# Optimization experiments

Measured on AMD Instinct MI355X. Metric: run time of the kernel, lower is better.

The kernel has to match this reference:

```python
import jax, jax.numpy as jnp
import numpy as np

EMBD = 1024
N_HEADS = 16
DK = EMBD // N_HEADS


def setup_inputs() -> dict:
    key = jax.random.key(0)
    ks = jax.random.split(key, 5)
    B, T = 2, 2048
    scale = 1.0 / np.sqrt(EMBD)
    x = jax.random.normal(ks[0], (B, T, EMBD), dtype=jnp.float32)
    W_qkv = jax.random.normal(ks[1], (EMBD, 3 * EMBD), dtype=jnp.float32) * scale
    b_qkv = jnp.zeros((3 * EMBD,), dtype=jnp.float32)
    W_proj = jax.random.normal(ks[2], (EMBD, EMBD), dtype=jnp.float32) * scale
    b_proj = jnp.zeros((EMBD,), dtype=jnp.float32)
    return {"x": x, "W_qkv": W_qkv, "b_qkv": b_qkv, "W_proj": W_proj, "b_proj": b_proj}


def reference(x, W_qkv, b_qkv, W_proj, b_proj):
    B, T, C = x.shape
    qkv = x @ W_qkv + b_qkv                      # [B, T, 3C]
    q, k, v = jnp.split(qkv, 3, axis=-1)
    # [B, H, T, dk]
    q = q.reshape(B, T, N_HEADS, DK).transpose(0, 2, 1, 3)
    k = k.reshape(B, T, N_HEADS, DK).transpose(0, 2, 1, 3)
    v = v.reshape(B, T, N_HEADS, DK).transpose(0, 2, 1, 3)
    att = jnp.einsum('bhqd,bhkd->bhqk', q, k) / np.sqrt(DK).astype(np.float32)
    causal = jnp.triu(jnp.full((T, T), -jnp.inf, dtype=att.dtype), k=1)
    att = jax.nn.softmax(att + causal, axis=-1)  # dropout p=0.0 -> identity
    y = jnp.einsum('bhqk,bhkd->bhqd', att, v)    # [B, H, T, dk]
    y = y.transpose(0, 2, 1, 3).reshape(B, T, C)
    y = y @ W_proj + b_proj
    return (y, (k, v))
```

## Files before the change

### kernel.cpp

```cpp
#include <hip/hip_runtime.h>
#include <hip/hip_bf16.h>

#define B_   2
#define T_   2048
#define C_   1024
#define H_   16
#define DK_  64

typedef __bf16 bf16x8 __attribute__((ext_vector_type(8)));
typedef __bf16 bf16x4v __attribute__((ext_vector_type(4)));
typedef float  f32x4  __attribute__((ext_vector_type(4)));
typedef unsigned short u16;
typedef u16 u16x4 __attribute__((ext_vector_type(4)));
typedef u16 u16x8 __attribute__((ext_vector_type(8)));

static __device__ __forceinline__ u16 f2bf(float f) {
    unsigned u = __float_as_uint(f);
    u += 0x7fffu + ((u >> 16) & 1u);
    return (u16)(u >> 16);
}
static __device__ __forceinline__ float bf2f(u16 h) {
    return __uint_as_float(((unsigned)h) << 16);
}

static __device__ __forceinline__ void async16(void* l, const void* g) {
    __builtin_amdgcn_global_load_lds(
        (const __attribute__((address_space(1))) unsigned int*)g,
        (__attribute__((address_space(3))) unsigned int*)l, 16, 0, 0);
}

__global__ __launch_bounds__(256) void pack_a_hl(const float* __restrict__ src, char* __restrict__ dst) {
    const int mt = blockIdx.x, kt = blockIdx.y, t = threadIdx.x;
    const int r = t >> 1, half = t & 1;
    const float* s = src + (size_t)(mt * 128 + r) * 1024 + kt * 32 + half * 16;
    float f[16];
    #pragma unroll
    for (int i = 0; i < 4; ++i) *(float4*)&f[i * 4] = ((const float4*)s)[i];
    u16 hi[16] __attribute__((aligned(16))), lo[16] __attribute__((aligned(16)));
    #pragma unroll
    for (int e = 0; e < 16; ++e) { hi[e] = f2bf(f[e]); lo[e] = f2bf(f[e] - bf2f(hi[e])); }
    char* tb = dst + ((size_t)mt * 32 + kt) * 16384;
    const int sw = (r & 7) << 4;
    #pragma unroll
    for (int j = 0; j < 2; ++j) {
        int g = half * 2 + j;
        *(u16x8*)(tb + ((r * 128 + g * 16) ^ sw))      = *(u16x8*)&hi[j * 8];
        *(u16x8*)(tb + ((r * 128 + 64 + g * 16) ^ sw)) = *(u16x8*)&lo[j * 8];
    }
}

__global__ __launch_bounds__(256) void pack_a_s(const float* __restrict__ src, char* __restrict__ dst) {
    const int mt = blockIdx.x, kt = blockIdx.y, t = threadIdx.x;
    const int r = t >> 1, half = t & 1;
    const float* s = src + (size_t)(mt * 128 + r) * 1024 + kt * 64 + half * 32;
    float f[32];
    #pragma unroll
    for (int i = 0; i < 8; ++i) *(float4*)&f[i * 4] = ((const float4*)s)[i];
    u16 hv[32] __attribute__((aligned(16)));
    #pragma unroll
    for (int e = 0; e < 32; ++e) hv[e] = f2bf(f[e]);
    char* tb = dst + ((size_t)mt * 16 + kt) * 16384;
    const int sw = (r & 7) << 4;
    #pragma unroll
    for (int j = 0; j < 4; ++j) {
        int g = half * 4 + j;
        *(u16x8*)(tb + ((r * 128 + g * 16) ^ sw)) = *(u16x8*)&hv[j * 8];
    }
}

template <int BKT>
__global__ __launch_bounds__(256) void pack_bt_hl(const float* __restrict__ W, char* __restrict__ dst,
                                                  int N, int nkt) {
    __shared__ float Ls[BKT][132];
    const int nt = blockIdx.x, kt = blockIdx.y, t = threadIdx.x;
    #pragma unroll
    for (int p = 0; p < BKT / 32; ++p) {
        int kr = p * 32 + (t >> 3), c8 = t & 7;
        const float* s = W + (size_t)(kt * BKT + kr) * N + nt * 128 + c8 * 16;
        #pragma unroll
        for (int i = 0; i < 4; ++i) *(float4*)&Ls[kr][c8 * 16 + i * 4] = ((const float4*)s)[i];
    }
    __syncthreads();
    const int nr = t >> 1, half = t & 1;
    constexpr int KH = BKT / 2;
    constexpr int ROWB = BKT * 4;
    constexpr int TILEB = 128 * ROWB;
    char* tb = dst + ((size_t)nt * nkt + kt) * TILEB;
    u16 hi[KH] __attribute__((aligned(16))), lo[KH] __attribute__((aligned(16)));
    #pragma unroll
    for (int e = 0; e < KH; ++e) {
        float x = Ls[half * KH + e][nr];
        hi[e] = f2bf(x); lo[e] = f2bf(x - bf2f(hi[e]));
    }
    const int sw = (nr & 7) << 4;
    #pragma unroll
    for (int j = 0; j < KH / 8; ++j) {
        int g = half * (KH / 8) + j;
        *(u16x8*)(tb + ((nr * ROWB + g * 16) ^ sw))            = *(u16x8*)&hi[j * 8];
        *(u16x8*)(tb + ((nr * ROWB + ROWB / 2 + g * 16) ^ sw)) = *(u16x8*)&lo[j * 8];
    }
}

__global__ __launch_bounds__(256) void kv_pack(
    const float* __restrict__ k_in, const float* __restrict__ v_in,
    char* __restrict__ kp, char* __restrict__ vp)
{
    __shared__ float Ls[64][68];
    const int bh = blockIdx.x, kt = blockIdx.y, t = threadIdx.x;
    const float* Kb = k_in + (size_t)bh * T_ * DK_ + (size_t)kt * 64 * DK_;
    const float* Vb = v_in + (size_t)bh * T_ * DK_ + (size_t)kt * 64 * DK_;
    char* ktb = kp + ((size_t)bh * 32 + kt) * 16384;
    char* vtb = vp + ((size_t)bh * 32 + kt) * 16384;
    const int row = t >> 2, qtr = t & 3;

    {
        float f[16];
        #pragma unroll
        for (int i = 0; i < 4; ++i)
            *(float4*)&f[i * 4] = ((const float4*)(Kb + (size_t)row * 64 + qtr * 16))[i];
        u16 hi[16] __attribute__((aligned(16))), lo[16] __attribute__((aligned(16)));
        #pragma unroll
        for (int e = 0; e < 16; ++e) { hi[e] = f2bf(f[e]); lo[e] = f2bf(f[e] - bf2f(hi[e])); }
        const int sw = (row & 7) << 4;
        *(u16x8*)(ktb + ((row * 128 + qtr * 32) ^ sw))             = *(u16x8*)&hi[0];
        *(u16x8*)(ktb + ((row * 128 + qtr * 32 + 16) ^ sw))        = *(u16x8*)&hi[8];
        *(u16x8*)(ktb + 8192 + ((row * 128 + qtr * 32) ^ sw))      = *(u16x8*)&lo[0];
        *(u16x8*)(ktb + 8192 + ((row * 128 + qtr * 32 + 16) ^ sw)) = *(u16x8*)&lo[8];
    }

    #pragma unroll
    for (int i = 0; i < 4; ++i)
        *(float4*)&Ls[row][qtr * 16 + i * 4] = ((const float4*)(Vb + (size_t)row * 64 + qtr * 16))[i];
    __syncthreads();
    {
        const int dd = t >> 2, tc2 = t & 3;
        float f[16];
        #pragma unroll
        for (int k = 0; k < 16; ++k) f[k] = Ls[tc2 * 16 + k][dd];
        u16 hi[16] __attribute__((aligned(16))), lo[16] __attribute__((aligned(16)));
        #pragma unroll
        for (int e = 0; e < 16; ++e) { hi[e] = f2bf(f[e]); lo[e] = f2bf(f[e] - bf2f(hi[e])); }
        const int sw = (dd & 7) << 4;
        *(u16x8*)(vtb + ((dd * 128 + tc2 * 32) ^ sw))             = *(u16x8*)&hi[0];
        *(u16x8*)(vtb + ((dd * 128 + tc2 * 32 + 16) ^ sw))        = *(u16x8*)&hi[8];
        *(u16x8*)(vtb + 8192 + ((dd * 128 + tc2 * 32) ^ sw))      = *(u16x8*)&lo[0];
        *(u16x8*)(vtb + 8192 + ((dd * 128 + tc2 * 32 + 16) ^ sw)) = *(u16x8*)&lo[8];
    }
}

__global__ __launch_bounds__(256, 2) void qkv_gemm_bf16(
    const char* __restrict__ xp, const char* __restrict__ wqp,
    const float* __restrict__ bqkv,
    float* __restrict__ qy, float* __restrict__ k_out, float* __restrict__ v_out)
{
    __shared__ __align__(16) char Alds[16384];
    __shared__ __align__(16) char Blds[16384];
    const int mt = blockIdx.x, nt = blockIdx.y;
    const int t = threadIdx.x, lane = t & 63, w = t >> 6;
    const int g = lane >> 4, r15 = lane & 15;
    const int wm = w >> 1, wn = w & 1;

    int aoff[4][2], boff[4][2];
    #pragma unroll
    for (int s = 0; s < 4; ++s) {
        int ar = wm * 64 + s * 16 + r15, sa = (ar & 7) << 4;
        aoff[s][0] = (ar * 128 + g * 16) ^ sa;
        aoff[s][1] = (ar * 128 + 64 + g * 16) ^ sa;
        int br = wn * 64 + s * 16 + r15, sb = (br & 7) << 4;
        boff[s][0] = (br * 128 + g * 16) ^ sb;
        boff[s][1] = (br * 128 + 64 + g * 16) ^ sb;
    }

    f32x4 acc[4][4];
    #pragma unroll
    for (int i = 0; i < 4; ++i)
        #pragma unroll
        for (int j = 0; j < 4; ++j) acc[i][j] = (f32x4){0.f, 0.f, 0.f, 0.f};

    const char* Abase = xp + (size_t)mt * 32 * 16384 + w * 4096 + lane * 16;
    const char* Bbase = wqp + (size_t)nt * 32 * 16384 + w * 4096 + lane * 16;
    char* la = Alds + w * 4096;
    char* lb = Blds + w * 4096;

    for (int kt = 0; kt < 32; ++kt) {
        #pragma unroll
        for (int i = 0; i < 4; ++i) {
            async16(la + i * 1024, Abase + kt * 16384 + i * 1024);
            async16(lb + i * 1024, Bbase + kt * 16384 + i * 1024);
        }
        __syncthreads();
        bf16x8 af[4][2], bf[4][2];
        #pragma unroll
        for (int s = 0; s < 4; ++s) {
            af[s][0] = *(const bf16x8*)(Alds + aoff[s][0]);
            af[s][1] = *(const bf16x8*)(Alds + aoff[s][1]);
            bf[s][0] = *(const bf16x8*)(Blds + boff[s][0]);
            bf[s][1] = *(const bf16x8*)(Blds + boff[s][1]);
        }
        #pragma unroll
        for (int i = 0; i < 4; ++i)
            #pragma unroll
            for (int j = 0; j < 4; ++j) {
                acc[i][j] = __builtin_amdgcn_mfma_f32_16x16x32_bf16(af[i][0], bf[j][0], acc[i][j], 0, 0, 0);
                acc[i][j] = __builtin_amdgcn_mfma_f32_16x16x32_bf16(af[i][0], bf[j][1], acc[i][j], 0, 0, 0);
                acc[i][j] = __builtin_amdgcn_mfma_f32_16x16x32_bf16(af[i][1], bf[j][0], acc[i][j], 0, 0, 0);
            }
        __syncthreads();
    }

    const int n0 = nt * 128;
    const int sec = n0 >> 10;
    float* kv = (sec == 1) ? k_out : v_out;
    #pragma unroll
    for (int i = 0; i < 4; ++i) {
        int mbase = mt * 128 + wm * 64 + i * 16 + g * 4;
        #pragma unroll
        for (int j = 0; j < 4; ++j) {
            int n = n0 + wn * 64 + j * 16 + r15;
            float bias = bqkv[n];
            int c = n & 1023;
            #pragma unroll
            for (int r = 0; r < 4; ++r) {
                int m = mbase + r;
                int bb = m >> 11, tt = m & 2047;
                float val = acc[i][j][r] + bias;
                if (sec == 0)
                    qy[((size_t)bb * T_ + tt) * C_ + c] = val;
                else
                    kv[(((size_t)bb * H_ + (c >> 6)) * T_ + tt) * DK_ + (c & 63)] = val;
            }
        }
    }
}

__global__ __launch_bounds__(256, 2) void proj_gemm_bf16(
    const char* __restrict__ yap, const char* __restrict__ wpp,
    const float* __restrict__ bp, float* __restrict__ y)
{
    __shared__ __align__(16) char Alds[16384];
    __shared__ __align__(16) char Blds[32768];
    const int mt = blockIdx.x, nt = blockIdx.y;
    const int t = threadIdx.x, lane = t & 63, w = t >> 6;
    const int g = lane >> 4, r15 = lane & 15;
    const int wm = w >> 1, wn = w & 1;

    int aoff[4][2], boffh[4][2], boffl[4][2];
    #pragma unroll
    for (int s = 0; s < 4; ++s) {
        int ar = wm * 64 + s * 16 + r15, sa = (ar & 7) << 4;
        int br = wn * 64 + s * 16 + r15, sb = (br & 7) << 4;
        #pragma unroll
        for (int kk = 0; kk < 2; ++kk) {
            aoff[s][kk]  = (ar * 128 + (kk * 4 + g) * 16) ^ sa;
            boffh[s][kk] = (br * 256 + (kk * 4 + g) * 16) ^ sb;
            boffl[s][kk] = (br * 256 + 128 + (kk * 4 + g) * 16) ^ sb;
        }
    }

    f32x4 acc[4][4];
    #pragma unroll
    for (int i = 0; i < 4; ++i)
        #pragma unroll
        for (int j = 0; j < 4; ++j) acc[i][j] = (f32x4){0.f, 0.f, 0.f, 0.f};

    const char* Abase = yap + (size_t)mt * 16 * 16384 + w * 4096 + lane * 16;
    const char* Bbase = wpp + (size_t)nt * 16 * 32768 + w * 8192 + lane * 16;
    char* la = Alds + w * 4096;
    char* lb = Blds + w * 8192;

    for (int kt = 0; kt < 16; ++kt) {
        #pragma unroll
        for (int i = 0; i < 4; ++i)
            async16(la + i * 1024, Abase + kt * 16384 + i * 1024);
        #pragma unroll
        for (int i = 0; i < 8; ++i)
            async16(lb + i * 1024, Bbase + kt * 32768 + i * 1024);
        __syncthreads();
        #pragma unroll
        for (int kk = 0; kk < 2; ++kk) {
            bf16x8 af[4], bh[4], bl[4];
            #pragma unroll
            for (int s = 0; s < 4; ++s) {
                af[s] = *(const bf16x8*)(Alds + aoff[s][kk]);
                bh[s] = *(const bf16x8*)(Blds + boffh[s][kk]);
                bl[s] = *(const bf16x8*)(Blds + boffl[s][kk]);
            }
            #pragma unroll
            for (int i = 0; i < 4; ++i)
                #pragma unroll
                for (int j = 0; j < 4; ++j) {
                    acc[i][j] = __builtin_amdgcn_mfma_f32_16x16x32_bf16(af[i], bh[j], acc[i][j], 0, 0, 0);
                    acc[i][j] = __builtin_amdgcn_mfma_f32_16x16x32_bf16(af[i], bl[j], acc[i][j], 0, 0, 0);
                }
        }
        __syncthreads();
    }

    #pragma unroll
    for (int i = 0; i < 4; ++i) {
        int mbase = mt * 128 + wm * 64 + i * 16 + g * 4;
        #pragma unroll
        for (int j = 0; j < 4; ++j) {
            int n = nt * 128 + wn * 64 + j * 16 + r15;
            float bias = bp[n];
            #pragma unroll
            for (int r = 0; r < 4; ++r)
                y[(size_t)(mbase + r) * 1024 + n] = acc[i][j][r] + bias;
        }
    }
}

#define PS_   0
#define KS_H  8192
#define KS_L  16384
#define VT_H  24576
#define VT_L  32768

__global__ __launch_bounds__(256) void attn_mfma_kernel(
    float* qyatt,
    const char* __restrict__ Kp,
    const char* __restrict__ Vp)
{
    __shared__ __align__(16) char lds[40960];

    const int bh   = blockIdx.x;
    const int qt   = 31 - (int)blockIdx.y;
    const int qb   = qt * 64;
    const int t    = threadIdx.x;
    const int lane = t & 63;
    const int w    = t >> 6;
    const int g    = lane >> 4;
    const int r15  = lane & 15;
    const int b    = bh >> 4, h = bh & 15;

    const float* Qb = qyatt + ((size_t)b * T_ + qb) * C_ + h * 64;
    const float QSCALE = 0.125f * 1.44269504088896f;

    #pragma unroll
    for (int di = 0; di < 4; ++di) {
        int fidx = di * 256 + t;
        int row  = fidx >> 4;
        int c4   = fidx & 15;
        float4 f = ((const float4*)(Qb + (size_t)row * C_))[c4];
        f.x *= QSCALE; f.y *= QSCALE; f.z *= QSCALE; f.w *= QSCALE;
        u16 h0 = f2bf(f.x), h1 = f2bf(f.y), h2 = f2bf(f.z), h3 = f2bf(f.w);
        u16 l0 = f2bf(f.x - bf2f(h0)), l1 = f2bf(f.y - bf2f(h1));
        u16 l2 = f2bf(f.z - bf2f(h2)), l3 = f2bf(f.w - bf2f(h3));
        int off = (row * 128 + c4 * 8) ^ ((row & 7) << 4);
        u16x4 hv = {h0, h1, h2, h3};
        u16x4 lv = {l0, l1, l2, l3};
        *(u16x4*)(lds + PS_  + off) = hv;
        *(u16x4*)(lds + KS_H + off) = lv;
    }
    __syncthreads();

    bf16x8 qfh[2], qfl[2];
    const int prow = w * 16 + r15;
    #pragma unroll
    for (int dc = 0; dc < 2; ++dc) {
        int off = (prow * 128 + dc * 64 + g * 16) ^ ((prow & 7) << 4);
        qfh[dc] = *(const bf16x8*)(lds + PS_  + off);
        qfl[dc] = *(const bf16x8*)(lds + KS_H + off);
    }

    f32x4 zero4 = {0.f, 0.f, 0.f, 0.f};
    f32x4 o[4];
    o[0] = zero4; o[1] = zero4; o[2] = zero4; o[3] = zero4;
    float mrun = -1e30f, lrun = 0.f;
    const int qglob = qb + w * 16 + r15;

    const int nt = qt + 1;
    for (int kt = 0; kt < nt; ++kt) {
        const int j0 = kt * 64;
        __syncthreads();
        {
            const char* Kg = Kp + ((size_t)bh * 32 + kt) * 16384 + w * 4096 + lane * 16;
            const char* Vg = Vp + ((size_t)bh * 32 + kt) * 16384 + w * 4096 + lane * 16;
            char* lk = lds + KS_H + w * 4096;
            char* lv = lds + VT_H + w * 4096;
            #pragma unroll
            for (int i = 0; i < 4; ++i) {
                async16(lk + i * 1024, Kg + i * 1024);
                async16(lv + i * 1024, Vg + i * 1024);
            }
        }
        __syncthreads();

        float sv[4][4];
        const bool diag = (kt == qt);
        #pragma unroll
        for (int st = 0; st < 4; ++st) {
            f32x4 acc = zero4;
            int krow = st * 16 + r15;
            #pragma unroll
            for (int dc = 0; dc < 2; ++dc) {
                int off = (krow * 128 + dc * 64 + g * 16) ^ ((krow & 7) << 4);
                bf16x8 kh = *(const bf16x8*)(lds + KS_H + off);
                bf16x8 kl = *(const bf16x8*)(lds + KS_L + off);
                acc = __builtin_amdgcn_mfma_f32_16x16x32_bf16(kh, qfh[dc], acc, 0, 0, 0);
                acc = __builtin_amdgcn_mfma_f32_16x16x32_bf16(kh, qfl[dc], acc, 0, 0, 0);
                acc = __builtin_amdgcn_mfma_f32_16x16x32_bf16(kl, qfh[dc], acc, 0, 0, 0);
            }
            #pragma unroll
            for (int r = 0; r < 4; ++r) {
                float x = acc[r];
                if (diag) {
                    int kg = j0 + st * 16 + g * 4 + r;
                    if (kg > qglob) x = -1e30f;
                }
                sv[st][r] = x;
            }
        }

        float tm = sv[0][0];
        #pragma unroll
        for (int st = 0; st < 4; ++st)
            #pragma unroll
            for (int r = 0; r < 4; ++r) tm = fmaxf(tm, sv[st][r]);
        tm = fmaxf(tm, __shfl_xor(tm, 16));
        tm = fmaxf(tm, __shfl_xor(tm, 32));
        if (__any(tm > mrun + 11.5f)) {
            float mnew = fmaxf(mrun, tm);
            float resc = exp2f(mrun - mnew);
            mrun = mnew;
            lrun *= resc;
            o[0] *= resc; o[1] *= resc; o[2] *= resc; o[3] *= resc;
        }

        float ps = 0.f;
        #pragma unroll
        for (int st = 0; st < 4; ++st)
            #pragma unroll
            for (int r = 0; r < 4; ++r) {
                float p = exp2f(sv[st][r] - mrun);
                sv[st][r] = p;
                ps += p;
            }
        ps += __shfl_xor(ps, 16);
        ps += __shfl_xor(ps, 32);
        lrun += ps;

        #pragma unroll
        for (int st = 0; st < 4; ++st) {
            bf16x4v pb = { (__bf16)sv[st][0], (__bf16)sv[st][1],
                           (__bf16)sv[st][2], (__bf16)sv[st][3] };
            int off = (prow * 128 + (st * 16 + g * 4) * 2) ^ ((prow & 7) << 4);
            *(bf16x4v*)(lds + PS_ + off) = pb;
        }

        bf16x8 pf[2];
        #pragma unroll
        for (int kc = 0; kc < 2; ++kc) {
            int off = (prow * 128 + kc * 64 + g * 16) ^ ((prow & 7) << 4);
            pf[kc] = *(const bf16x8*)(lds + PS_ + off);
        }
        #pragma unroll
        for (int dt = 0; dt < 4; ++dt) {
            int vrow = dt * 16 + r15;
            #pragma unroll
            for (int kc = 0; kc < 2; ++kc) {
                int off = (vrow * 128 + kc * 64 + g * 16) ^ ((vrow & 7) << 4);
                bf16x8 vh = *(const bf16x8*)(lds + VT_H + off);
                bf16x8 vl = *(const bf16x8*)(lds + VT_L + off);
                o[dt] = __builtin_amdgcn_mfma_f32_16x16x32_bf16(vh, pf[kc], o[dt], 0, 0, 0);
                o[dt] = __builtin_amdgcn_mfma_f32_16x16x32_bf16(vl, pf[kc], o[dt], 0, 0, 0);
            }
        }
    }

    const float inv = 1.f / lrun;
    float* yo = qyatt + ((size_t)b * T_ + qglob) * C_ + h * DK_;
    #pragma unroll
    for (int dt = 0; dt < 4; ++dt)
        #pragma unroll
        for (int r = 0; r < 4; ++r)
            yo[dt * 16 + g * 4 + r] = o[dt][r] * inv;
}

extern "C" void kernel_launch(void* const* d_in, const int* in_sizes, int n_in,
                              void* d_out, int out_size, void* d_ws, size_t ws_size,
                              hipStream_t stream) {
    const float* x     = (const float*)d_in[0];
    const float* Wqkv  = (const float*)d_in[1];
    const float* bqkv  = (const float*)d_in[2];
    const float* Wproj = (const float*)d_in[3];
    const float* bproj = (const float*)d_in[4];

    float* y     = (float*)d_out;
    float* k_out = y + (size_t)4194304;
    float* v_out = y + (size_t)8388608;

    char* ws = (char*)d_ws;
    char* xp  = ws;
    char* wqp = ws + ((size_t)16 << 20);
    char* Kp  = ws;
    char* Vp  = ws + ((size_t)16 << 20);
    char* yap = ws;
    char* wpp = ws + ((size_t)8 << 20);

    pack_a_hl     <<<dim3(32, 32), 256, 0, stream>>>(x, xp);
    pack_bt_hl<32><<<dim3(24, 32), 256, 0, stream>>>(Wqkv, wqp, 3072, 32);
    qkv_gemm_bf16 <<<dim3(32, 24), 256, 0, stream>>>(xp, wqp, bqkv, y, k_out, v_out);
    kv_pack       <<<dim3(32, 32), 256, 0, stream>>>(k_out, v_out, Kp, Vp);
    attn_mfma_kernel<<<dim3(32, 32), 256, 0, stream>>>(y, Kp, Vp);
    pack_a_s      <<<dim3(32, 16), 256, 0, stream>>>(y, yap);
    pack_bt_hl<64><<<dim3(8, 16), 256, 0, stream>>>(Wproj, wpp, 1024, 16);
    proj_gemm_bf16<<<dim3(32, 8), 256, 0, stream>>>(yap, wpp, bproj, y);
}
```

Before: 298.7 us.

## Double-buffer K/V tiles and widen attention blocks to 128 query rows

The attention kernel now processes 128 query rows per block with 8 waves, so each K/V tile loaded into LDS is shared by twice as many queries. K/V tiles are double-buffered: the next tile's async copy is issued before computing on the current one, leaving one barrier per iteration instead of two. Query-tile ordering is interleaved so heavy and light causal tiles are mixed across the grid. In exchange, LDS use doubles to 80 KB per block, which may limit occupancy, and waves past the diagonal sit idle through the remaining iterations.

```diff
diff --git a/kernel.cpp b/kernel.cpp
--- a/kernel.cpp
+++ b/kernel.cpp
@@ -310,22 +310,23 @@
     }
 }
 
-#define PS_   0
-#define KS_H  8192
-#define KS_L  16384
-#define VT_H  24576
-#define VT_L  32768
-
-__global__ __launch_bounds__(256) void attn_mfma_kernel(
+#define PS_    0
+#define BUF0_  16384
+#define BUF1_  49152
+#define QT_H   16384
+#define QT_L   32768
+
+__global__ __launch_bounds__(512) void attn_mfma_kernel(
     float* qyatt,
     const char* __restrict__ Kp,
     const char* __restrict__ Vp)
 {
-    __shared__ __align__(16) char lds[40960];
+    __shared__ __align__(16) char lds[81920];
 
     const int bh   = blockIdx.x;
-    const int qt   = 31 - (int)blockIdx.y;
-    const int qb   = qt * 64;
+    const int by   = blockIdx.y;
+    const int qt   = (by < 8) ? (15 - by) : (by - 8);
+    const int qb   = qt * 128;
     const int t    = threadIdx.x;
     const int lane = t & 63;
     const int w    = t >> 6;
@@ -338,7 +339,7 @@
 
     #pragma unroll
     for (int di = 0; di < 4; ++di) {
-        int fidx = di * 256 + t;
+        int fidx = di * 512 + t;
         int row  = fidx >> 4;
         int c4   = fidx & 15;
         float4 f = ((const float4*)(Qb + (size_t)row * C_))[c4];
@@ -349,8 +350,8 @@
         int off = (row * 128 + c4 * 8) ^ ((row & 7) << 4);
         u16x4 hv = {h0, h1, h2, h3};
         u16x4 lv = {l0, l1, l2, l3};
-        *(u16x4*)(lds + PS_  + off) = hv;
-        *(u16x4*)(lds + KS_H + off) = lv;
+        *(u16x4*)(lds + QT_H + off) = hv;
+        *(u16x4*)(lds + QT_L + off) = lv;
     }
     __syncthreads();
 
@@ -359,113 +360,129 @@
     #pragma unroll
     for (int dc = 0; dc < 2; ++dc) {
         int off = (prow * 128 + dc * 64 + g * 16) ^ ((prow & 7) << 4);
-        qfh[dc] = *(const bf16x8*)(lds + PS_  + off);
-        qfl[dc] = *(const bf16x8*)(lds + KS_H + off);
-    }
+        qfh[dc] = *(const bf16x8*)(lds + QT_H + off);
+        qfl[dc] = *(const bf16x8*)(lds + QT_L + off);
+    }
+    __syncthreads();
 
     f32x4 zero4 = {0.f, 0.f, 0.f, 0.f};
     f32x4 o[4];
     o[0] = zero4; o[1] = zero4; o[2] = zero4; o[3] = zero4;
     float mrun = -1e30f, lrun = 0.f;
-    const int qglob = qb + w * 16 + r15;
-
-    const int nt = qt + 1;
+    const int qglob = qb + prow;
+    const int ktd   = (qb + w * 16) >> 6;
+    const int nt    = qt * 2 + 2;
+
+    const char* KVg[2] = {
+        Kp + (size_t)bh * 32 * 16384 + (w & 3) * 4096 + lane * 16,
+        Vp + (size_t)bh * 32 * 16384 + (w & 3) * 4096 + lane * 16 };
+    const char* gsrc = KVg[w >> 2];
+    char* ldst0 = lds + BUF0_ + (w >> 2) * 16384 + (w & 3) * 4096;
+    char* ldst1 = lds + BUF1_ + (w >> 2) * 16384 + (w & 3) * 4096;
+
+    #pragma unroll
+    for (int i = 0; i < 4; ++i)
+        async16(ldst0 + i * 1024, gsrc + i * 1024);
+    __syncthreads();
+
     for (int kt = 0; kt < nt; ++kt) {
-        const int j0 = kt * 64;
+        if (kt + 1 < nt) {
+            char* ld = ((kt + 1) & 1) ? ldst1 : ldst0;
+            const char* gs = gsrc + (size_t)(kt + 1) * 16384;
+            #pragma unroll
+            for (int i = 0; i < 4; ++i)
+                async16(ld + i * 1024, gs + i * 1024);
+        }
+
+        if (kt <= ktd) {
+            const char* KB = lds + ((kt & 1) ? BUF1_ : BUF0_);
+            const char* KH = KB,         * KL = KB + 8192;
+            const char* VH = KB + 16384, * VL = KB + 24576;
+            const int j0 = kt * 64;
+            const bool diag = (kt == ktd);
+
+            float sv[4][4];
+            #pragma unroll
+            for (int st = 0; st < 4; ++st) {
+                f32x4 acc = zero4;
+                int krow = st * 16 + r15;
+                #pragma unroll
+                for (int dc = 0; dc < 2; ++dc) {
+                    int off = (krow * 128 + dc * 64 + g * 16) ^ ((krow & 7) << 4);
+                    bf16x8 kh = *(const bf16x8*)(KH + off);
+                    bf16x8 kl = *(const bf16x8*)(KL + off);
+                    acc = __builtin_amdgcn_mfma_f32_16x16x32_bf16(kh, qfh[dc], acc, 0, 0, 0);
+                    acc = __builtin_amdgcn_mfma_f32_16x16x32_bf16(kh, qfl[dc], acc, 0, 0, 0);
+                    acc = __builtin_amdgcn_mfma_f32_16x16x32_bf16(kl, qfh[dc], acc, 0, 0, 0);
+                }
+                #pragma unroll
+                for (int r = 0; r < 4; ++r) {
+                    float x = acc[r];
+                    if (diag) {
+                        int kg = j0 + st * 16 + g * 4 + r;
+                        if (kg > qglob) x = -1e30f;
+                    }
+                    sv[st][r] = x;
+                }
+            }
+
+            float tm = sv[0][0];
+            #pragma unroll
+            for (int st = 0; st < 4; ++st)
+                #pragma unroll
+                for (int r = 0; r < 4; ++r) tm = fmaxf(tm, sv[st][r]);
+            tm = fmaxf(tm, __shfl_xor(tm, 16));
+            tm = fmaxf(tm, __shfl_xor(tm, 32));
+            if (__any(tm > mrun + 11.5f)) {
+                float mnew = fmaxf(mrun, tm);
+                float resc = exp2f(mrun - mnew);
+                mrun = mnew;
+                lrun *= resc;
+                o[0] *= resc; o[1] *= resc; o[2] *= resc; o[3] *= resc;
+            }
+
+            float ps = 0.f;
+            #pragma unroll
+            for (int st = 0; st < 4; ++st)
+                #pragma unroll
+                for (int r = 0; r < 4; ++r) {
+                    float p = exp2f(sv[st][r] - mrun);
+                    sv[st][r] = p;
+                    ps += p;
+                }
+            ps += __shfl_xor(ps, 16);
+            ps += __shfl_xor(ps, 32);
+            lrun += ps;
+
+            #pragma unroll
+            for (int st = 0; st < 4; ++st) {
+                bf16x4v pb = { (__bf16)sv[st][0], (__bf16)sv[st][1],
+                               (__bf16)sv[st][2], (__bf16)sv[st][3] };
+                int off = (prow * 128 + (st * 16 + g * 4) * 2) ^ ((prow & 7) << 4);
+                *(bf16x4v*)(lds + PS_ + off) = pb;
+            }
+
+            bf16x8 pf[2];
+            #pragma unroll
+            for (int kc = 0; kc < 2; ++kc) {
+                int off = (prow * 128 + kc * 64 + g * 16) ^ ((prow & 7) << 4);
+                pf[kc] = *(const bf16x8*)(lds + PS_ + off);
+            }
+            #pragma unroll
+            for (int dt = 0; dt < 4; ++dt) {
+                int vrow = dt * 16 + r15;
+                #pragma unroll
+                for (int kc = 0; kc < 2; ++kc) {
+                    int off = (vrow * 128 + kc * 64 + g * 16) ^ ((vrow & 7) << 4);
+                    bf16x8 vh = *(const bf16x8*)(VH + off);
+                    bf16x8 vl = *(const bf16x8*)(VL + off);
+                    o[dt] = __builtin_amdgcn_mfma_f32_16x16x32_bf16(vh, pf[kc], o[dt], 0, 0, 0);
+                    o[dt] = __builtin_amdgcn_mfma_f32_16x16x32_bf16(vl, pf[kc], o[dt], 0, 0, 0);
+                }
+            }
+        }
+
         __syncthreads();
-        {
-            const char* Kg = Kp + ((size_t)bh * 32 + kt) * 16384 + w * 4096 + lane * 16;
-            const char* Vg = Vp + ((size_t)bh * 32 + kt) * 16384 + w * 4096 + lane * 16;
-            char* lk = lds + KS_H + w * 4096;
-            char* lv = lds + VT_H + w * 4096;
-            #pragma unroll
-            for (int i = 0; i < 4; ++i) {
-                async16(lk + i * 1024, Kg + i * 1024);
-                async16(lv + i * 1024, Vg + i * 1024);
-            }
-        }
-        __syncthreads();
-
-        float sv[4][4];
-        const bool diag = (kt == qt);
-        #pragma unroll
-        for (int st = 0; st < 4; ++st) {
-            f32x4 acc = zero4;
-            int krow = st * 16 + r15;
-            #pragma unroll
-            for (int dc = 0; dc < 2; ++dc) {
-                int off = (krow * 128 + dc * 64 + g * 16) ^ ((krow & 7) << 4);
-                bf16x8 kh = *(const bf16x8*)(lds + KS_H + off);
-                bf16x8 kl = *(const bf16x8*)(lds + KS_L + off);
-                acc = __builtin_amdgcn_mfma_f32_16x16x32_bf16(kh, qfh[dc], acc, 0, 0, 0);
-                acc = __builtin_amdgcn_mfma_f32_16x16x32_bf16(kh, qfl[dc], acc, 0, 0, 0);
-                acc = __builtin_amdgcn_mfma_f32_16x16x32_bf16(kl, qfh[dc], acc, 0, 0, 0);
-            }
-            #pragma unroll
-            for (int r = 0; r < 4; ++r) {
-                float x = acc[r];
-                if (diag) {
-                    int kg = j0 + st * 16 + g * 4 + r;
-                    if (kg > qglob) x = -1e30f;
-                }
-                sv[st][r] = x;
-            }
-        }
-
-        float tm = sv[0][0];
-        #pragma unroll
-        for (int st = 0; st < 4; ++st)
-            #pragma unroll
-            for (int r = 0; r < 4; ++r) tm = fmaxf(tm, sv[st][r]);
-        tm = fmaxf(tm, __shfl_xor(tm, 16));
-        tm = fmaxf(tm, __shfl_xor(tm, 32));
-        if (__any(tm > mrun + 11.5f)) {
-            float mnew = fmaxf(mrun, tm);
-            float resc = exp2f(mrun - mnew);
-            mrun = mnew;
-            lrun *= resc;
-            o[0] *= resc; o[1] *= resc; o[2] *= resc; o[3] *= resc;
-        }
-
-        float ps = 0.f;
-        #pragma unroll
-        for (int st = 0; st < 4; ++st)
-            #pragma unroll
-            for (int r = 0; r < 4; ++r) {
-                float p = exp2f(sv[st][r] - mrun);
-                sv[st][r] = p;
-                ps += p;
-            }
-        ps += __shfl_xor(ps, 16);
-        ps += __shfl_xor(ps, 32);
-        lrun += ps;
-
-        #pragma unroll
-        for (int st = 0; st < 4; ++st) {
-            bf16x4v pb = { (__bf16)sv[st][0], (__bf16)sv[st][1],
-                           (__bf16)sv[st][2], (__bf16)sv[st][3] };
-            int off = (prow * 128 + (st * 16 + g * 4) * 2) ^ ((prow & 7) << 4);
-            *(bf16x4v*)(lds + PS_ + off) = pb;
-        }
-
-        bf16x8 pf[2];
-        #pragma unroll
-        for (int kc = 0; kc < 2; ++kc) {
-            int off = (prow * 128 + kc * 64 + g * 16) ^ ((prow & 7) << 4);
-            pf[kc] = *(const bf16x8*)(lds + PS_ + off);
-        }
-        #pragma unroll
-        for (int dt = 0; dt < 4; ++dt) {
-            int vrow = dt * 16 + r15;
-            #pragma unroll
-            for (int kc = 0; kc < 2; ++kc) {
-                int off = (vrow * 128 + kc * 64 + g * 16) ^ ((vrow & 7) << 4);
-                bf16x8 vh = *(const bf16x8*)(lds + VT_H + off);
-                bf16x8 vl = *(const bf16x8*)(lds + VT_L + off);
-                o[dt] = __builtin_amdgcn_mfma_f32_16x16x32_bf16(vh, pf[kc], o[dt], 0, 0, 0);
-                o[dt] = __builtin_amdgcn_mfma_f32_16x16x32_bf16(vl, pf[kc], o[dt], 0, 0, 0);
-            }
-        }
     }
 
     const float inv = 1.f / lrun;
@@ -502,7 +519,7 @@
     pack_bt_hl<32><<<dim3(24, 32), 256, 0, stream>>>(Wqkv, wqp, 3072, 32);
     qkv_gemm_bf16 <<<dim3(32, 24), 256, 0, stream>>>(xp, wqp, bqkv, y, k_out, v_out);
     kv_pack       <<<dim3(32, 32), 256, 0, stream>>>(k_out, v_out, Kp, Vp);
-    attn_mfma_kernel<<<dim3(32, 32), 256, 0, stream>>>(y, Kp, Vp);
+    attn_mfma_kernel<<<dim3(32, 16), 512, 0, stream>>>(y, Kp, Vp);
     pack_a_s      <<<dim3(32, 16), 256, 0, stream>>>(y, yap);
     pack_bt_hl<64><<<dim3(8, 16), 256, 0, stream>>>(Wproj, wpp, 1024, 16);
     proj_gemm_bf16<<<dim3(32, 8), 256, 0, stream>>>(yap, wpp, bproj, y);
```

After: 288.2 us. 3.5% less time.
